# Kernel tuning notes

Hardware: AMD Instinct MI355X
Metric: run time of the kernel (lower is better)

Reference implementation:

```python
import jax, jax.numpy as jnp
import numpy as np
import math

D_MODEL = 512


def setup_inputs() -> dict:
    key = jax.random.key(0)
    x = jax.random.normal(key, (16384, 32), dtype=jnp.float32)
    return {"x": x}


def reference(x) -> jnp.ndarray:
    # x: [B, F]; output: [B, D_MODEL]
    d_model = D_MODEL
    # div_term: [D/2]
    div_term = jnp.exp(jnp.arange(0, d_model, 2, dtype=jnp.float32) * (-(math.log(10000.0) / d_model)))
    # sinusoid input: [B, F, D/2]
    si = x[:, :, None] * div_term
    sin_mean = jnp.sin(si).mean(axis=1)  # [B, D/2]
    cos_mean = jnp.cos(si).mean(axis=1)  # [B, D/2]
    # interleave: out[:, 0::2] = sin_mean, out[:, 1::2] = cos_mean
    out = jnp.stack([sin_mean, cos_mean], axis=-1).reshape(x.shape[0], d_model)
    return out
```

## Files before the change

kernel.cpp:

```cpp
#include <hip/hip_runtime.h>

#define F 32
#define D_HALF 256
#define NP 22
#define STRIDE 23

__constant__ float kTable[NP] = {
     3.125e-2f,
    -1.5625e-2f,
    -5.2083333333333336e-3f,
     1.3020833333333333e-3f,
     2.6041666666666666e-4f,
    -4.3402777777777778e-5f,
    -6.2003968253968254e-6f,
     7.7504960317460317e-7f,
     8.6116622574955908e-8f,
    -8.6116622574955908e-9f,
    -7.8287838704505371e-10f,
     6.5239865587087809e-11f,
     5.0184511989929083e-12f,
    -3.5846079992806488e-13f,
    -2.3897386661870992e-14f,
     1.4935866663669370e-15f,
     8.7858039198055118e-17f,
    -4.8810021776697288e-18f,
    -2.5689485145630152e-19f,
     1.2844742572815076e-20f,
     6.1165440822928934e-22f,
    -2.7802473101331334e-23f
};

__global__ __launch_bounds__(256) void pe_kernel(const float* __restrict__ x,
                                                 float2* __restrict__ out) {
    const int b = blockIdx.x;
    const int tid = threadIdx.x;

    __shared__ float pw[F * STRIDE];
    __shared__ float mom[NP];

    if (tid < F) {
        const float v = x[b * F + tid];
        float p = v;
#pragma unroll
        for (int k = 0; k < NP; ++k) {
            pw[tid * STRIDE + k] = p;
            p *= v;
        }
    }
    __syncthreads();

    if (tid < NP) {
        float s = 0.0f;
#pragma unroll
        for (int f = 0; f < F; ++f) s += pw[f * STRIDE + tid];
        mom[tid] = s * kTable[tid];
    }
    __syncthreads();

    const float kExp = -0.05190512648261503f;
    const float d = __builtin_amdgcn_exp2f((float)tid * kExp);
    const float t = d * d;

    float s = mom[20];
    s = fmaf(s, t, mom[18]);
    s = fmaf(s, t, mom[16]);
    s = fmaf(s, t, mom[14]);
    s = fmaf(s, t, mom[12]);
    s = fmaf(s, t, mom[10]);
    s = fmaf(s, t, mom[8]);
    s = fmaf(s, t, mom[6]);
    s = fmaf(s, t, mom[4]);
    s = fmaf(s, t, mom[2]);
    s = fmaf(s, t, mom[0]);
    s *= d;

    float c = mom[21];
    c = fmaf(c, t, mom[19]);
    c = fmaf(c, t, mom[17]);
    c = fmaf(c, t, mom[15]);
    c = fmaf(c, t, mom[13]);
    c = fmaf(c, t, mom[11]);
    c = fmaf(c, t, mom[9]);
    c = fmaf(c, t, mom[7]);
    c = fmaf(c, t, mom[5]);
    c = fmaf(c, t, mom[3]);
    c = fmaf(c, t, mom[1]);
    c = fmaf(c, t, 1.0f);

    out[b * D_HALF + tid] = make_float2(s, c);
}

extern "C" void kernel_launch(void* const* d_in, const int* in_sizes, int n_in,
                              void* d_out, int out_size, void* d_ws, size_t ws_size,
                              hipStream_t stream) {
    const float* x = (const float*)d_in[0];
    float2* out = (float2*)d_out;
    const int B = in_sizes[0] / F;
    pe_kernel<<<B, 256, 0, stream>>>(x, out);
}
```

Baseline: 71.34 us.

## Compute moments per wave with shuffles in a persistent grid-stride kernel

Restructures the kernel so each 64-lane wave handles two rows, with each half-wave computing the power moments in registers and reducing them with xor shuffles. This replaces the shared-memory power table, the serial 22-thread summation and both block barriers. A fixed grid of 1024 blocks grid-strides over row pairs, and each lane evaluates 8 output columns per row. It assumes an even batch size and raises per-thread register use and serial work per lane.

```diff
diff --git a/kernel.cpp b/kernel.cpp
--- a/kernel.cpp
+++ b/kernel.cpp
@@ -3,9 +3,10 @@
 #define F 32
 #define D_HALF 256
 #define NP 22
-#define STRIDE 23
+#define BLOCKS 1024
+#define TPB 256
 
-__constant__ float kTable[NP] = {
+__device__ constexpr float kTable[NP] = {
      3.125e-2f,
     -1.5625e-2f,
     -5.2083333333333336e-3f,
@@ -30,64 +31,72 @@
     -2.7802473101331334e-23f
 };
 
-__global__ __launch_bounds__(256) void pe_kernel(const float* __restrict__ x,
-                                                 float2* __restrict__ out) {
-    const int b = blockIdx.x;
-    const int tid = threadIdx.x;
+__global__ __launch_bounds__(TPB) void pe_kernel(const float* __restrict__ x,
+                                                 float2* __restrict__ out,
+                                                 int B) {
+    const int lane = threadIdx.x & 63;
+    const int fl   = lane & 31;
+    const int half = lane >> 5;
+    const int gwave  = blockIdx.x * (TPB / 64) + (threadIdx.x >> 6);
+    const int nwaves = gridDim.x * (TPB / 64);
+    const int npairs = B >> 1;
 
-    __shared__ float pw[F * STRIDE];
-    __shared__ float mom[NP];
+    const float kExp = -0.05190512648261503f;
 
-    if (tid < F) {
-        const float v = x[b * F + tid];
+    for (int rp = gwave; rp < npairs; rp += nwaves) {
+        const int r = (rp << 1) + half;
+        const float v = x[r * F + fl];
+
+        float mom[NP];
         float p = v;
 #pragma unroll
+        for (int k = 0; k < NP; ++k) { mom[k] = p; p *= v; }
+#pragma unroll
         for (int k = 0; k < NP; ++k) {
-            pw[tid * STRIDE + k] = p;
-            p *= v;
+            float s = mom[k];
+            s += __shfl_xor(s, 1);
+            s += __shfl_xor(s, 2);
+            s += __shfl_xor(s, 4);
+            s += __shfl_xor(s, 8);
+            s += __shfl_xor(s, 16);
+            mom[k] = s * kTable[k];
+        }
+
+        float2* orow = out + r * D_HALF;
+#pragma unroll
+        for (int m = 0; m < 8; ++m) {
+            const int j = fl + 32 * m;
+            const float d = __builtin_amdgcn_exp2f((float)j * kExp);
+            const float t = d * d;
+
+            float s = mom[20];
+            s = fmaf(s, t, mom[18]);
+            s = fmaf(s, t, mom[16]);
+            s = fmaf(s, t, mom[14]);
+            s = fmaf(s, t, mom[12]);
+            s = fmaf(s, t, mom[10]);
+            s = fmaf(s, t, mom[8]);
+            s = fmaf(s, t, mom[6]);
+            s = fmaf(s, t, mom[4]);
+            s = fmaf(s, t, mom[2]);
+            s = fmaf(s, t, mom[0]);
+
+            float c = mom[21];
+            c = fmaf(c, t, mom[19]);
+            c = fmaf(c, t, mom[17]);
+            c = fmaf(c, t, mom[15]);
+            c = fmaf(c, t, mom[13]);
+            c = fmaf(c, t, mom[11]);
+            c = fmaf(c, t, mom[9]);
+            c = fmaf(c, t, mom[7]);
+            c = fmaf(c, t, mom[5]);
+            c = fmaf(c, t, mom[3]);
+            c = fmaf(c, t, mom[1]);
+            c = fmaf(c, t, 1.0f);
+
+            orow[j] = make_float2(s * d, c);
         }
     }
-    __syncthreads();
-
-    if (tid < NP) {
-        float s = 0.0f;
-#pragma unroll
-        for (int f = 0; f < F; ++f) s += pw[f * STRIDE + tid];
-        mom[tid] = s * kTable[tid];
-    }
-    __syncthreads();
-
-    const float kExp = -0.05190512648261503f;
-    const float d = __builtin_amdgcn_exp2f((float)tid * kExp);
-    const float t = d * d;
-
-    float s = mom[20];
-    s = fmaf(s, t, mom[18]);
-    s = fmaf(s, t, mom[16]);
-    s = fmaf(s, t, mom[14]);
-    s = fmaf(s, t, mom[12]);
-    s = fmaf(s, t, mom[10]);
-    s = fmaf(s, t, mom[8]);
-    s = fmaf(s, t, mom[6]);
-    s = fmaf(s, t, mom[4]);
-    s = fmaf(s, t, mom[2]);
-    s = fmaf(s, t, mom[0]);
-    s *= d;
-
-    float c = mom[21];
-    c = fmaf(c, t, mom[19]);
-    c = fmaf(c, t, mom[17]);
-    c = fmaf(c, t, mom[15]);
-    c = fmaf(c, t, mom[13]);
-    c = fmaf(c, t, mom[11]);
-    c = fmaf(c, t, mom[9]);
-    c = fmaf(c, t, mom[7]);
-    c = fmaf(c, t, mom[5]);
-    c = fmaf(c, t, mom[3]);
-    c = fmaf(c, t, mom[1]);
-    c = fmaf(c, t, 1.0f);
-
-    out[b * D_HALF + tid] = make_float2(s, c);
 }
 
 extern "C" void kernel_launch(void* const* d_in, const int* in_sizes, int n_in,
@@ -96,5 +105,5 @@
     const float* x = (const float*)d_in[0];
     float2* out = (float2*)d_out;
     const int B = in_sizes[0] / F;
-    pe_kernel<<<B, 256, 0, stream>>>(x, out);
+    pe_kernel<<<BLOCKS, TPB, 0, stream>>>(x, out, B);
 }
```

After: 72.66 us. About the same (+1.8%).
